# Kernel tuning notes

Hardware: AMD Instinct MI355X
Metric: run time of the kernel (lower is better)

Reference implementation:

```python
import jax, jax.numpy as jnp
import numpy as np

# dMoE config (matches init_kwargs): D=1024, GLU ffn F=2816 (int(2*4096/3) rounded up to 256),
# E=8 experts, top_k=2, erf-GELU activation, normalize_expert_weights=0 (skip), bias added to output.
D = 1024
F = 2816
E = 8
TOP_K = 2


def setup_inputs() -> dict:
    key = jax.random.key(0)
    ks = jax.random.split(key, 6)
    std = 0.02
    x = jax.random.normal(ks[0], (2, 2048, D), dtype=jnp.float32)
    router_w = jax.random.normal(ks[1], (D, E), dtype=jnp.float32) * std
    w1 = jax.random.normal(ks[2], (E, D, F), dtype=jnp.float32) * std
    v1 = jax.random.normal(ks[3], (E, D, F), dtype=jnp.float32) * std
    w2 = jax.random.normal(ks[4], (E, F, D), dtype=jnp.float32) * std
    bias = jnp.zeros((D,), dtype=jnp.float32)
    return {"x": x, "router_w": router_w, "w1": w1, "v1": v1, "w2": w2, "bias": bias}


def reference(x, router_w, w1, v1, w2, bias):
    B, S, d = x.shape
    xt = x.reshape(B * S, d)                       # [T, D] tokens
    # Router: linear -> softmax over experts -> top-k (no weight renormalization, p=0).
    scores = jax.nn.softmax(xt @ router_w, axis=-1)          # [T, E]
    expert_weights, expert_idx = jax.lax.top_k(scores, TOP_K)  # [T, k]
    # Dropless MoE == dense per-expert GLU MLP combined with top-k weights
    # (non-selected experts get weight 0, mathematically identical to dispatch/combine).
    h = jax.nn.gelu(jnp.einsum('td,edf->tef', xt, w1), approximate=False) \
        * jnp.einsum('td,edf->tef', xt, v1)                   # [T, E, F]
    y = jnp.einsum('tef,efd->ted', h, w2)                     # [T, E, D]
    yk = jnp.take_along_axis(y, expert_idx[:, :, None], axis=1)  # [T, k, D]
    out = jnp.sum(expert_weights[:, :, None] * yk, axis=1) + bias
    return out.reshape(B, S, d)
```

## Files before the change

kernel.cpp:

```cpp
#include <hip/hip_runtime.h>
#include <hip/hip_bf16.h>
#include <math.h>

#define D_DIM 1024
#define F_DIM 2816
#define E_NUM 8

#define BM 128
#define BK 64

typedef __attribute__((ext_vector_type(4))) float f32x4;
typedef __attribute__((ext_vector_type(8))) short short8;

__device__ __forceinline__ unsigned short f2bf(float f) {
    unsigned u = __float_as_uint(f);
    u = (u + 0x7FFFu + ((u >> 16) & 1u)) >> 16;
    return (unsigned short)u;
}

__device__ __forceinline__ float gelu_erf(float z) {
    return 0.5f * z * (1.0f + erff(z * 0.70710678118654752f));
}

__device__ __forceinline__ int swz(int row, int kb) {
    return row * 128 + (kb ^ ((row & 7) << 4));
}

__device__ __forceinline__ uint4 pack8(const unsigned short* h) {
    uint4 r;
    r.x = (unsigned)h[0] | ((unsigned)h[1] << 16);
    r.y = (unsigned)h[2] | ((unsigned)h[3] << 16);
    r.z = (unsigned)h[4] | ((unsigned)h[5] << 16);
    r.w = (unsigned)h[6] | ((unsigned)h[7] << 16);
    return r;
}

__device__ __forceinline__ void gload16(const void* g, void* l) {
    __builtin_amdgcn_global_load_lds(
        (const __attribute__((address_space(1))) unsigned int*)g,
        (__attribute__((address_space(3))) unsigned int*)l,
        16, 0, 0);
}

__global__ __launch_bounds__(256) void transpose_cvt_kernel(
    const float* __restrict__ src, unsigned short* __restrict__ dst, int R, int C)
{
    __shared__ float tile[64][65];
    int e = blockIdx.z;
    const float* s = src + (size_t)e * R * C;
    unsigned short* d = dst + (size_t)e * R * C;
    int c0 = blockIdx.x * 64;
    int r0 = blockIdx.y * 64;
    int tid = threadIdx.x;
#pragma unroll
    for (int i = 0; i < 4; ++i) {
        int idx = tid + 256 * i;
        int r = idx >> 4, cc = (idx & 15) * 4;
        float4 v = *(const float4*)(s + (size_t)(r0 + r) * C + c0 + cc);
        tile[r][cc] = v.x; tile[r][cc + 1] = v.y; tile[r][cc + 2] = v.z; tile[r][cc + 3] = v.w;
    }
    __syncthreads();
#pragma unroll
    for (int i = 0; i < 2; ++i) {
        int idx = tid + 256 * i;
        int c = idx >> 3, rr = (idx & 7) * 8;
        unsigned short h[8];
#pragma unroll
        for (int j = 0; j < 8; ++j) h[j] = f2bf(tile[rr + j][c]);
        *(uint4*)(d + (size_t)(c0 + c) * R + r0 + rr) = pack8(h);
    }
}

__global__ __launch_bounds__(64) void router_kernel(
    const float* __restrict__ x, const float* __restrict__ rw,
    unsigned short* __restrict__ xbf, int* __restrict__ tk_idx,
    float* __restrict__ tk_w, int* __restrict__ counts)
{
    int t = blockIdx.x;
    int lane = threadIdx.x;
    const float* xr = x + (size_t)t * D_DIM;
    float acc[E_NUM];
#pragma unroll
    for (int e = 0; e < E_NUM; ++e) acc[e] = 0.f;
#pragma unroll
    for (int i = 0; i < D_DIM / 64; ++i) {
        int d = lane + 64 * i;
        float xv = xr[d];
        xbf[(size_t)t * D_DIM + d] = f2bf(xv);
        const float* rp = rw + (size_t)d * E_NUM;
#pragma unroll
        for (int e = 0; e < E_NUM; ++e) acc[e] += xv * rp[e];
    }
#pragma unroll
    for (int e = 0; e < E_NUM; ++e) {
#pragma unroll
        for (int s = 32; s > 0; s >>= 1) acc[e] += __shfl_xor(acc[e], s, 64);
    }
    float mx = acc[0];
#pragma unroll
    for (int e = 1; e < E_NUM; ++e) mx = fmaxf(mx, acc[e]);
    float p[E_NUM], se = 0.f;
#pragma unroll
    for (int e = 0; e < E_NUM; ++e) { p[e] = expf(acc[e] - mx); se += p[e]; }
    float inv = 1.f / se;
    int e1 = 0;
#pragma unroll
    for (int e = 1; e < E_NUM; ++e) if (p[e] > p[e1]) e1 = e;
    int e2 = (e1 == 0) ? 1 : 0;
#pragma unroll
    for (int e = 0; e < E_NUM; ++e) if (e != e1 && p[e] > p[e2]) e2 = e;
    if (lane == 0) {
        tk_idx[2 * t] = e1; tk_idx[2 * t + 1] = e2;
        tk_w[2 * t] = p[e1] * inv; tk_w[2 * t + 1] = p[e2] * inv;
        atomicAdd(&counts[e1], 1);
        atomicAdd(&counts[e2], 1);
    }
}

__global__ void scan_kernel(const int* __restrict__ counts, int* __restrict__ offsets,
                            int* __restrict__ tile_e, int* __restrict__ tile_row,
                            int* __restrict__ n_mt)
{
    if (threadIdx.x != 0) return;
    int off = 0, nt = 0;
    for (int e = 0; e < E_NUM; ++e) {
        offsets[e] = off;
        int ne = counts[e];
        int nti = (ne + BM - 1) / BM;
        for (int i = 0; i < nti; ++i) { tile_e[nt] = e; tile_row[nt] = off + i * BM; ++nt; }
        off += ne;
    }
    offsets[E_NUM] = off;
    *n_mt = nt;
}

__global__ __launch_bounds__(256) void compact_kernel(
    const int* __restrict__ tk_idx, const int* __restrict__ offsets,
    int* __restrict__ pair_token, int* __restrict__ pair_pos, int T)
{
    int e = blockIdx.x;
    int tid = threadIdx.x;
    __shared__ int s[256];
    __shared__ int running;
    if (tid == 0) running = 0;
    __syncthreads();
    int base0 = offsets[e];
    for (int base = 0; base < T; base += 256) {
        int t = base + tid;
        int flag = 0, slot = -1;
        if (t < T) {
            int i0 = tk_idx[2 * t], i1 = tk_idx[2 * t + 1];
            slot = (i0 == e) ? 0 : ((i1 == e) ? 1 : -1);
            flag = (slot >= 0) ? 1 : 0;
        }
        s[tid] = flag;
        __syncthreads();
        for (int d = 1; d < 256; d <<= 1) {
            int v = (tid >= d) ? s[tid - d] : 0;
            __syncthreads();
            s[tid] += v;
            __syncthreads();
        }
        int total = s[255];
        int run = running;
        if (flag) {
            int pos = base0 + run + s[tid] - 1;
            pair_token[pos] = t;
            pair_pos[2 * t + slot] = pos;
        }
        __syncthreads();
        if (tid == 0) running += total;
        __syncthreads();
    }
}

__global__ __launch_bounds__(512) void gemm1_glu_kernel(
    const unsigned short* __restrict__ xbf,
    const unsigned short* __restrict__ w1t, const unsigned short* __restrict__ v1t,
    const int* __restrict__ pair_token, const int* __restrict__ offsets,
    const int* __restrict__ tile_e, const int* __restrict__ tile_row,
    const int* __restrict__ n_mt,
    unsigned short* __restrict__ hbf)
{
    int mt = blockIdx.x;
    if (mt >= *n_mt) return;
    int e = tile_e[mt];
    int row0 = tile_row[mt];
    int end = offsets[e + 1];
    int n0 = blockIdx.y * 64;

    __shared__ __align__(16) unsigned short As[BM * BK];
    __shared__ __align__(16) unsigned short B0s[64 * BK];
    __shared__ __align__(16) unsigned short B1s[64 * BK];

    int tid = threadIdx.x;
    int lane = tid & 63;
    int wid = tid >> 6;
    int wr = wid >> 1, wc = wid & 1;
    int sub = lane >> 3;
    int srcoff = (((lane & 7) ^ sub) << 4);

    const unsigned short* W0 = w1t + (size_t)e * D_DIM * F_DIM;
    const unsigned short* W1 = v1t + (size_t)e * D_DIM * F_DIM;

    const char* aptr[2];
#pragma unroll
    for (int i = 0; i < 2; ++i) {
        int row = (wid * 2 + i) * 8 + sub;
        int p = row0 + row;
        if (p >= end) p = end - 1;
        aptr[i] = (const char*)(xbf + (size_t)pair_token[p] * D_DIM) + srcoff;
    }
    int nb = wid * 8 + sub;
    const char* b0ptr = (const char*)(W0 + (size_t)(n0 + nb) * D_DIM) + srcoff;
    const char* b1ptr = (const char*)(W1 + (size_t)(n0 + nb) * D_DIM) + srcoff;

    f32x4 acc[2][2][2];
#pragma unroll
    for (int a = 0; a < 2; ++a)
#pragma unroll
        for (int m = 0; m < 2; ++m)
#pragma unroll
            for (int n = 0; n < 2; ++n) acc[a][m][n] = (f32x4){0.f, 0.f, 0.f, 0.f};

    auto STAGE = [&]() {
#pragma unroll
        for (int i = 0; i < 2; ++i) {
            gload16(aptr[i], (char*)As + (wid * 2 + i) * 1024);
            aptr[i] += 128;
        }
        gload16(b0ptr, (char*)B0s + wid * 1024);
        b0ptr += 128;
        gload16(b1ptr, (char*)B1s + wid * 1024);
        b1ptr += 128;
    };

    const int NT = D_DIM / BK;
    for (int kt = 0; kt < NT; ++kt) {
        STAGE();
        __syncthreads();
#pragma unroll
        for (int kk = 0; kk < 2; ++kk) {
            int kb = kk * 64 + (lane >> 4) * 16;
            short8 af[2];
#pragma unroll
            for (int m = 0; m < 2; ++m) {
                int row = wr * 32 + m * 16 + (lane & 15);
                af[m] = *(const short8*)((char*)As + swz(row, kb));
            }
            short8 bf0[2], bf1[2];
#pragma unroll
            for (int n = 0; n < 2; ++n) {
                int rn = wc * 32 + n * 16 + (lane & 15);
                bf0[n] = *(const short8*)((char*)B0s + swz(rn, kb));
                bf1[n] = *(const short8*)((char*)B1s + swz(rn, kb));
            }
#pragma unroll
            for (int m = 0; m < 2; ++m)
#pragma unroll
                for (int n = 0; n < 2; ++n) {
                    acc[0][m][n] = __builtin_amdgcn_mfma_f32_16x16x32_bf16(af[m], bf0[n], acc[0][m][n], 0, 0, 0);
                    acc[1][m][n] = __builtin_amdgcn_mfma_f32_16x16x32_bf16(af[m], bf1[n], acc[1][m][n], 0, 0, 0);
                }
        }
        __syncthreads();
    }
#pragma unroll
    for (int m = 0; m < 2; ++m) {
#pragma unroll
        for (int j = 0; j < 4; ++j) {
            int rl = wr * 32 + m * 16 + (lane >> 4) * 4 + j;
            int p = row0 + rl;
            if (p < end) {
#pragma unroll
                for (int n = 0; n < 2; ++n) {
                    float z1 = acc[0][m][n][j];
                    float z2 = acc[1][m][n][j];
                    float hv = gelu_erf(z1) * z2;
                    hbf[(size_t)p * F_DIM + n0 + wc * 32 + n * 16 + (lane & 15)] = f2bf(hv);
                }
            }
        }
    }
}

__global__ __launch_bounds__(512) void gemm2_kernel(
    const unsigned short* __restrict__ hbf,
    const unsigned short* __restrict__ w2t,
    const int* __restrict__ offsets,
    const int* __restrict__ tile_e, const int* __restrict__ tile_row,
    const int* __restrict__ n_mt,
    float* __restrict__ ypair)
{
    int mt = blockIdx.x;
    if (mt >= *n_mt) return;
    int e = tile_e[mt];
    int row0 = tile_row[mt];
    int end = offsets[e + 1];
    int n0 = blockIdx.y * 128;

    __shared__ __align__(16) unsigned short As[BM * BK];
    __shared__ __align__(16) unsigned short Bs[128 * BK];

    int tid = threadIdx.x;
    int lane = tid & 63;
    int wid = tid >> 6;
    int wr = wid >> 2, wc = wid & 3;
    int sub = lane >> 3;
    int srcoff = (((lane & 7) ^ sub) << 4);

    const unsigned short* W = w2t + (size_t)e * D_DIM * F_DIM;

    const char* aptr[2];
#pragma unroll
    for (int i = 0; i < 2; ++i) {
        int row = (wid * 2 + i) * 8 + sub;
        int p = row0 + row;
        if (p >= end) p = end - 1;
        aptr[i] = (const char*)(hbf + (size_t)p * F_DIM) + srcoff;
    }
    const char* bptr[2];
#pragma unroll
    for (int i = 0; i < 2; ++i) {
        int n = (wid * 2 + i) * 8 + sub;
        bptr[i] = (const char*)(W + (size_t)(n0 + n) * F_DIM) + srcoff;
    }

    f32x4 acc[4][2];
#pragma unroll
    for (int m = 0; m < 4; ++m)
#pragma unroll
        for (int n = 0; n < 2; ++n) acc[m][n] = (f32x4){0.f, 0.f, 0.f, 0.f};

    auto STAGE = [&]() {
#pragma unroll
        for (int i = 0; i < 2; ++i) {
            gload16(aptr[i], (char*)As + (wid * 2 + i) * 1024);
            aptr[i] += 128;
            gload16(bptr[i], (char*)Bs + (wid * 2 + i) * 1024);
            bptr[i] += 128;
        }
    };

    const int NT = F_DIM / BK;
    for (int kt = 0; kt < NT; ++kt) {
        STAGE();
        __syncthreads();
#pragma unroll
        for (int kk = 0; kk < 2; ++kk) {
            int kb = kk * 64 + (lane >> 4) * 16;
            short8 af[4];
#pragma unroll
            for (int m = 0; m < 4; ++m) {
                int row = wr * 64 + m * 16 + (lane & 15);
                af[m] = *(const short8*)((char*)As + swz(row, kb));
            }
            short8 bfr[2];
#pragma unroll
            for (int n = 0; n < 2; ++n) {
                int rn = wc * 32 + n * 16 + (lane & 15);
                bfr[n] = *(const short8*)((char*)Bs + swz(rn, kb));
            }
#pragma unroll
            for (int m = 0; m < 4; ++m)
#pragma unroll
                for (int n = 0; n < 2; ++n)
                    acc[m][n] = __builtin_amdgcn_mfma_f32_16x16x32_bf16(af[m], bfr[n], acc[m][n], 0, 0, 0);
        }
        __syncthreads();
    }
#pragma unroll
    for (int m = 0; m < 4; ++m) {
#pragma unroll
        for (int j = 0; j < 4; ++j) {
            int rl = wr * 64 + m * 16 + (lane >> 4) * 4 + j;
            int p = row0 + rl;
            if (p < end) {
#pragma unroll
                for (int n = 0; n < 2; ++n)
                    ypair[(size_t)p * D_DIM + n0 + wc * 32 + n * 16 + (lane & 15)] = acc[m][n][j];
            }
        }
    }
}

__global__ __launch_bounds__(256) void combine_kernel(
    const float* __restrict__ ypair, const int* __restrict__ pair_pos,
    const float* __restrict__ tk_w, const float* __restrict__ bias,
    float* __restrict__ out, int total)
{
    int idx = blockIdx.x * 256 + threadIdx.x;
    if (idx >= total) return;
    int t = idx >> 10;
    int d = idx & (D_DIM - 1);
    int p0 = pair_pos[2 * t], p1 = pair_pos[2 * t + 1];
    float r = bias[d] + tk_w[2 * t] * ypair[(size_t)p0 * D_DIM + d]
                      + tk_w[2 * t + 1] * ypair[(size_t)p1 * D_DIM + d];
    out[idx] = r;
}

__global__ void ws_too_small_kernel(float* out, int n) {
    int i = blockIdx.x * 256 + threadIdx.x;
    if (i < n) out[i] = 12345.0f;
}

extern "C" void kernel_launch(void* const* d_in, const int* in_sizes, int n_in,
                              void* d_out, int out_size, void* d_ws, size_t ws_size,
                              hipStream_t stream) {
    const float* x    = (const float*)d_in[0];
    const float* rw   = (const float*)d_in[1];
    const float* w1   = (const float*)d_in[2];
    const float* v1   = (const float*)d_in[3];
    const float* w2   = (const float*)d_in[4];
    const float* bias = (const float*)d_in[5];
    float* out = (float*)d_out;

    int T = in_sizes[0] / D_DIM;
    int P = 2 * T;
    int maxMT = P / BM + E_NUM;

    char* p = (char*)d_ws;
    char* ws_end = p + ws_size;
    auto alloc = [&](size_t bytes) {
        char* r = p;
        p += (bytes + 255) & ~(size_t)255;
        return r;
    };
    unsigned short* xbf   = (unsigned short*)alloc((size_t)T * D_DIM * 2);
    int*   tk_idx     = (int*)alloc((size_t)T * 2 * 4);
    float* tk_w       = (float*)alloc((size_t)T * 2 * 4);
    int*   counts     = (int*)alloc(E_NUM * 4);
    int*   offsets    = (int*)alloc((E_NUM + 1) * 4);
    int*   tile_e     = (int*)alloc(maxMT * 4);
    int*   tile_row   = (int*)alloc(maxMT * 4);
    int*   n_mt       = (int*)alloc(4);
    int*   pair_token = (int*)alloc((size_t)P * 4);
    int*   pair_pos   = (int*)alloc((size_t)P * 4);
    unsigned short* hbf = (unsigned short*)alloc((size_t)P * F_DIM * 2);
    float* ypair      = (float*)alloc((size_t)P * D_DIM * 4);
    unsigned short* w1t = (unsigned short*)alloc((size_t)E_NUM * D_DIM * F_DIM * 2);
    unsigned short* v1t = (unsigned short*)alloc((size_t)E_NUM * D_DIM * F_DIM * 2);
    unsigned short* w2t = (unsigned short*)alloc((size_t)E_NUM * D_DIM * F_DIM * 2);

    if (p > ws_end) {
        ws_too_small_kernel<<<(out_size + 255) / 256, 256, 0, stream>>>(out, out_size);
        return;
    }

    hipMemsetAsync(counts, 0, E_NUM * 4, stream);
    transpose_cvt_kernel<<<dim3(F_DIM / 64, D_DIM / 64, E_NUM), 256, 0, stream>>>(w1, w1t, D_DIM, F_DIM);
    transpose_cvt_kernel<<<dim3(F_DIM / 64, D_DIM / 64, E_NUM), 256, 0, stream>>>(v1, v1t, D_DIM, F_DIM);
    transpose_cvt_kernel<<<dim3(D_DIM / 64, F_DIM / 64, E_NUM), 256, 0, stream>>>(w2, w2t, F_DIM, D_DIM);
    router_kernel<<<T, 64, 0, stream>>>(x, rw, xbf, tk_idx, tk_w, counts);
    scan_kernel<<<1, 64, 0, stream>>>(counts, offsets, tile_e, tile_row, n_mt);
    compact_kernel<<<E_NUM, 256, 0, stream>>>(tk_idx, offsets, pair_token, pair_pos, T);
    gemm1_glu_kernel<<<dim3(maxMT, F_DIM / 64), 512, 0, stream>>>(
        xbf, w1t, v1t, pair_token, offsets, tile_e, tile_row, n_mt, hbf);
    gemm2_kernel<<<dim3(maxMT, D_DIM / 128), 512, 0, stream>>>(
        hbf, w2t, offsets, tile_e, tile_row, n_mt, ypair);
    combine_kernel<<<(T * D_DIM + 255) / 256, 256, 0, stream>>>(
        ypair, pair_pos, tk_w, bias, out, T * D_DIM);
}
```

Before: 456.2 us.

## Double-buffer GEMM LDS tiles and fuse top-k combine into GEMM2 via atomics

Both expert GEMM kernels now double-buffer their shared-memory tiles. The next K-slice load is issued before computing on the current one, which removes one barrier per iteration and overlaps global loads with MFMA work. The separate combine kernel and the ypair buffer are replaced: a bias-init kernel writes the bias into the output, and GEMM2 scales each result by its routing weight and atomically adds it into the token's output row. This removes the fp32 ypair write and read-back, at the cost of doubled LDS use (possibly lower occupancy) and global float atomics with a nondeterministic summation order.

```diff
diff --git a/kernel.cpp b/kernel.cpp
--- a/kernel.cpp
+++ b/kernel.cpp
@@ -136,7 +136,8 @@
 
 __global__ __launch_bounds__(256) void compact_kernel(
     const int* __restrict__ tk_idx, const int* __restrict__ offsets,
-    int* __restrict__ pair_token, int* __restrict__ pair_pos, int T)
+    const float* __restrict__ tk_w,
+    int* __restrict__ pair_token, float* __restrict__ pair_w, int T)
 {
     int e = blockIdx.x;
     int tid = threadIdx.x;
@@ -166,12 +167,21 @@
         if (flag) {
             int pos = base0 + run + s[tid] - 1;
             pair_token[pos] = t;
-            pair_pos[2 * t + slot] = pos;
+            pair_w[pos] = tk_w[2 * t + slot];
         }
         __syncthreads();
         if (tid == 0) running += total;
         __syncthreads();
     }
+}
+
+__global__ __launch_bounds__(256) void bias_init_kernel(
+    const float* __restrict__ bias, float* __restrict__ out, int total4)
+{
+    int idx = blockIdx.x * 256 + threadIdx.x;
+    if (idx >= total4) return;
+    int d4 = idx & (D_DIM / 4 - 1);
+    ((float4*)out)[idx] = ((const float4*)bias)[d4];
 }
 
 __global__ __launch_bounds__(512) void gemm1_glu_kernel(
@@ -189,9 +199,9 @@
     int end = offsets[e + 1];
     int n0 = blockIdx.y * 64;
 
-    __shared__ __align__(16) unsigned short As[BM * BK];
-    __shared__ __align__(16) unsigned short B0s[64 * BK];
-    __shared__ __align__(16) unsigned short B1s[64 * BK];
+    __shared__ __align__(16) unsigned short As[2][BM * BK];
+    __shared__ __align__(16) unsigned short B0s[2][64 * BK];
+    __shared__ __align__(16) unsigned short B1s[2][64 * BK];
 
     int tid = threadIdx.x;
     int lane = tid & 63;
@@ -223,22 +233,27 @@
 #pragma unroll
             for (int n = 0; n < 2; ++n) acc[a][m][n] = (f32x4){0.f, 0.f, 0.f, 0.f};
 
-    auto STAGE = [&]() {
+    auto STAGE = [&](int buf) {
 #pragma unroll
         for (int i = 0; i < 2; ++i) {
-            gload16(aptr[i], (char*)As + (wid * 2 + i) * 1024);
+            gload16(aptr[i], (char*)As[buf] + (wid * 2 + i) * 1024);
             aptr[i] += 128;
         }
-        gload16(b0ptr, (char*)B0s + wid * 1024);
+        gload16(b0ptr, (char*)B0s[buf] + wid * 1024);
         b0ptr += 128;
-        gload16(b1ptr, (char*)B1s + wid * 1024);
+        gload16(b1ptr, (char*)B1s[buf] + wid * 1024);
         b1ptr += 128;
     };
 
+    STAGE(0);
     const int NT = D_DIM / BK;
+    int cur = 0;
     for (int kt = 0; kt < NT; ++kt) {
-        STAGE();
         __syncthreads();
+        if (kt + 1 < NT) STAGE(cur ^ 1);
+        const char* Ab = (const char*)As[cur];
+        const char* B0b = (const char*)B0s[cur];
+        const char* B1b = (const char*)B1s[cur];
 #pragma unroll
         for (int kk = 0; kk < 2; ++kk) {
             int kb = kk * 64 + (lane >> 4) * 16;
@@ -246,14 +261,14 @@
 #pragma unroll
             for (int m = 0; m < 2; ++m) {
                 int row = wr * 32 + m * 16 + (lane & 15);
-                af[m] = *(const short8*)((char*)As + swz(row, kb));
+                af[m] = *(const short8*)(Ab + swz(row, kb));
             }
             short8 bf0[2], bf1[2];
 #pragma unroll
             for (int n = 0; n < 2; ++n) {
                 int rn = wc * 32 + n * 16 + (lane & 15);
-                bf0[n] = *(const short8*)((char*)B0s + swz(rn, kb));
-                bf1[n] = *(const short8*)((char*)B1s + swz(rn, kb));
+                bf0[n] = *(const short8*)(B0b + swz(rn, kb));
+                bf1[n] = *(const short8*)(B1b + swz(rn, kb));
             }
 #pragma unroll
             for (int m = 0; m < 2; ++m)
@@ -263,7 +278,7 @@
                     acc[1][m][n] = __builtin_amdgcn_mfma_f32_16x16x32_bf16(af[m], bf1[n], acc[1][m][n], 0, 0, 0);
                 }
         }
-        __syncthreads();
+        cur ^= 1;
     }
 #pragma unroll
     for (int m = 0; m < 2; ++m) {
@@ -290,7 +305,8 @@
     const int* __restrict__ offsets,
     const int* __restrict__ tile_e, const int* __restrict__ tile_row,
     const int* __restrict__ n_mt,
-    float* __restrict__ ypair)
+    const int* __restrict__ pair_token, const float* __restrict__ pair_w,
+    float* __restrict__ out)
 {
     int mt = blockIdx.x;
     if (mt >= *n_mt) return;
@@ -299,8 +315,8 @@
     int end = offsets[e + 1];
     int n0 = blockIdx.y * 128;
 
-    __shared__ __align__(16) unsigned short As[BM * BK];
-    __shared__ __align__(16) unsigned short Bs[128 * BK];
+    __shared__ __align__(16) unsigned short As[2][BM * BK];
+    __shared__ __align__(16) unsigned short Bs[2][128 * BK];
 
     int tid = threadIdx.x;
     int lane = tid & 63;
@@ -332,20 +348,24 @@
 #pragma unroll
         for (int n = 0; n < 2; ++n) acc[m][n] = (f32x4){0.f, 0.f, 0.f, 0.f};
 
-    auto STAGE = [&]() {
+    auto STAGE = [&](int buf) {
 #pragma unroll
         for (int i = 0; i < 2; ++i) {
-            gload16(aptr[i], (char*)As + (wid * 2 + i) * 1024);
+            gload16(aptr[i], (char*)As[buf] + (wid * 2 + i) * 1024);
             aptr[i] += 128;
-            gload16(bptr[i], (char*)Bs + (wid * 2 + i) * 1024);
+            gload16(bptr[i], (char*)Bs[buf] + (wid * 2 + i) * 1024);
             bptr[i] += 128;
         }
     };
 
+    STAGE(0);
     const int NT = F_DIM / BK;
+    int cur = 0;
     for (int kt = 0; kt < NT; ++kt) {
-        STAGE();
         __syncthreads();
+        if (kt + 1 < NT) STAGE(cur ^ 1);
+        const char* Ab = (const char*)As[cur];
+        const char* Bb = (const char*)Bs[cur];
 #pragma unroll
         for (int kk = 0; kk < 2; ++kk) {
             int kb = kk * 64 + (lane >> 4) * 16;
@@ -353,13 +373,13 @@
 #pragma unroll
             for (int m = 0; m < 4; ++m) {
                 int row = wr * 64 + m * 16 + (lane & 15);
-                af[m] = *(const short8*)((char*)As + swz(row, kb));
+                af[m] = *(const short8*)(Ab + swz(row, kb));
             }
             short8 bfr[2];
 #pragma unroll
             for (int n = 0; n < 2; ++n) {
                 int rn = wc * 32 + n * 16 + (lane & 15);
-                bfr[n] = *(const short8*)((char*)Bs + swz(rn, kb));
+                bfr[n] = *(const short8*)(Bb + swz(rn, kb));
             }
 #pragma unroll
             for (int m = 0; m < 4; ++m)
@@ -367,7 +387,7 @@
                 for (int n = 0; n < 2; ++n)
                     acc[m][n] = __builtin_amdgcn_mfma_f32_16x16x32_bf16(af[m], bfr[n], acc[m][n], 0, 0, 0);
         }
-        __syncthreads();
+        cur ^= 1;
     }
 #pragma unroll
     for (int m = 0; m < 4; ++m) {
@@ -376,27 +396,15 @@
             int rl = wr * 64 + m * 16 + (lane >> 4) * 4 + j;
             int p = row0 + rl;
             if (p < end) {
+                int t = pair_token[p];
+                float w = pair_w[p];
+                float* orow = out + (size_t)t * D_DIM + n0 + wc * 32 + (lane & 15);
 #pragma unroll
                 for (int n = 0; n < 2; ++n)
-                    ypair[(size_t)p * D_DIM + n0 + wc * 32 + n * 16 + (lane & 15)] = acc[m][n][j];
-            }
-        }
-    }
-}
-
-__global__ __launch_bounds__(256) void combine_kernel(
-    const float* __restrict__ ypair, const int* __restrict__ pair_pos,
-    const float* __restrict__ tk_w, const float* __restrict__ bias,
-    float* __restrict__ out, int total)
-{
-    int idx = blockIdx.x * 256 + threadIdx.x;
-    if (idx >= total) return;
-    int t = idx >> 10;
-    int d = idx & (D_DIM - 1);
-    int p0 = pair_pos[2 * t], p1 = pair_pos[2 * t + 1];
-    float r = bias[d] + tk_w[2 * t] * ypair[(size_t)p0 * D_DIM + d]
-                      + tk_w[2 * t + 1] * ypair[(size_t)p1 * D_DIM + d];
-    out[idx] = r;
+                    atomicAdd(orow + n * 16, w * acc[m][n][j]);
+            }
+        }
+    }
 }
 
 __global__ void ws_too_small_kernel(float* out, int n) {
@@ -435,9 +443,8 @@
     int*   tile_row   = (int*)alloc(maxMT * 4);
     int*   n_mt       = (int*)alloc(4);
     int*   pair_token = (int*)alloc((size_t)P * 4);
-    int*   pair_pos   = (int*)alloc((size_t)P * 4);
+    float* pair_w     = (float*)alloc((size_t)P * 4);
     unsigned short* hbf = (unsigned short*)alloc((size_t)P * F_DIM * 2);
-    float* ypair      = (float*)alloc((size_t)P * D_DIM * 4);
     unsigned short* w1t = (unsigned short*)alloc((size_t)E_NUM * D_DIM * F_DIM * 2);
     unsigned short* v1t = (unsigned short*)alloc((size_t)E_NUM * D_DIM * F_DIM * 2);
     unsigned short* w2t = (unsigned short*)alloc((size_t)E_NUM * D_DIM * F_DIM * 2);
@@ -453,11 +460,10 @@
     transpose_cvt_kernel<<<dim3(D_DIM / 64, F_DIM / 64, E_NUM), 256, 0, stream>>>(w2, w2t, F_DIM, D_DIM);
     router_kernel<<<T, 64, 0, stream>>>(x, rw, xbf, tk_idx, tk_w, counts);
     scan_kernel<<<1, 64, 0, stream>>>(counts, offsets, tile_e, tile_row, n_mt);
-    compact_kernel<<<E_NUM, 256, 0, stream>>>(tk_idx, offsets, pair_token, pair_pos, T);
+    compact_kernel<<<E_NUM, 256, 0, stream>>>(tk_idx, offsets, tk_w, pair_token, pair_w, T);
     gemm1_glu_kernel<<<dim3(maxMT, F_DIM / 64), 512, 0, stream>>>(
         xbf, w1t, v1t, pair_token, offsets, tile_e, tile_row, n_mt, hbf);
+    bias_init_kernel<<<(T * D_DIM / 4 + 255) / 256, 256, 0, stream>>>(bias, out, T * D_DIM / 4);
     gemm2_kernel<<<dim3(maxMT, D_DIM / 128), 512, 0, stream>>>(
-        hbf, w2t, offsets, tile_e, tile_row, n_mt, ypair);
-    combine_kernel<<<(T * D_DIM + 255) / 256, 256, 0, stream>>>(
-        ypair, pair_pos, tk_w, bias, out, T * D_DIM);
-}
+        hbf, w2t, offsets, tile_e, tile_row, n_mt, pair_token, pair_w, out);
+}
```

Measured after the change: 493.2 us. +8.1%, slower.

## Enlarge MoE GEMM tiles to 256 rows with double-buffered LDS and XCD-aware block remap

Applied to the files above, without the earlier changes.

Both grouped GEMMs move to 256-row M tiles. The GLU GEMM now computes a 128-wide combined w1/v1 N strip per block, and each wave holds a larger accumulator set. LDS is double-buffered, with loads issued two stages ahead and explicit vmcnt waits and barriers replacing the single-buffer syncthreads loop. Block indices are remapped so consecutive logical tiles go to the same XCD to improve L2 reuse. The aim is more reuse per load and latency hiding, at the cost of higher register and LDS pressure (lower occupancy) and more wasted work on partially filled expert tiles.

```diff
diff --git a/kernel.cpp b/kernel.cpp
--- a/kernel.cpp
+++ b/kernel.cpp
@@ -6,7 +6,7 @@
 #define F_DIM 2816
 #define E_NUM 8
 
-#define BM 128
+#define BM 256
 #define BK 64
 
 typedef __attribute__((ext_vector_type(4))) float f32x4;
@@ -182,102 +182,125 @@
     const int* __restrict__ n_mt,
     unsigned short* __restrict__ hbf)
 {
-    int mt = blockIdx.x;
+    __shared__ __align__(16) unsigned short As[2][256 * BK];
+    __shared__ __align__(16) unsigned short Bs[2][256 * BK];
+
+    int flat = blockIdx.x + gridDim.x * blockIdx.y;
+    int nwg = gridDim.x * gridDim.y;
+    int L = (flat & 7) * (nwg >> 3) + (flat >> 3);
+    int mt = L % gridDim.x;
+    int strip = L / gridDim.x;
     if (mt >= *n_mt) return;
     int e = tile_e[mt];
     int row0 = tile_row[mt];
     int end = offsets[e + 1];
-    int n0 = blockIdx.y * 64;
-
-    __shared__ __align__(16) unsigned short As[BM * BK];
-    __shared__ __align__(16) unsigned short B0s[64 * BK];
-    __shared__ __align__(16) unsigned short B1s[64 * BK];
+    int n0 = strip * 128;
 
     int tid = threadIdx.x;
     int lane = tid & 63;
     int wid = tid >> 6;
-    int wr = wid >> 1, wc = wid & 1;
+    int wr = wid >> 2, wc = wid & 3;
     int sub = lane >> 3;
     int srcoff = (((lane & 7) ^ sub) << 4);
 
     const unsigned short* W0 = w1t + (size_t)e * D_DIM * F_DIM;
     const unsigned short* W1 = v1t + (size_t)e * D_DIM * F_DIM;
 
-    const char* aptr[2];
-#pragma unroll
-    for (int i = 0; i < 2; ++i) {
-        int row = (wid * 2 + i) * 8 + sub;
-        int p = row0 + row;
+    const char* aptr[4];
+#pragma unroll
+    for (int i = 0; i < 4; ++i) {
+        int r = (wid * 4 + i) * 8 + sub;
+        int p = row0 + r;
         if (p >= end) p = end - 1;
         aptr[i] = (const char*)(xbf + (size_t)pair_token[p] * D_DIM) + srcoff;
     }
-    int nb = wid * 8 + sub;
-    const char* b0ptr = (const char*)(W0 + (size_t)(n0 + nb) * D_DIM) + srcoff;
-    const char* b1ptr = (const char*)(W1 + (size_t)(n0 + nb) * D_DIM) + srcoff;
-
-    f32x4 acc[2][2][2];
-#pragma unroll
-    for (int a = 0; a < 2; ++a)
-#pragma unroll
-        for (int m = 0; m < 2; ++m)
-#pragma unroll
-            for (int n = 0; n < 2; ++n) acc[a][m][n] = (f32x4){0.f, 0.f, 0.f, 0.f};
-
-    auto STAGE = [&]() {
-#pragma unroll
-        for (int i = 0; i < 2; ++i) {
-            gload16(aptr[i], (char*)As + (wid * 2 + i) * 1024);
+    const char* bptr[4];
+#pragma unroll
+    for (int i = 0; i < 4; ++i) {
+        int gb = wid * 4 + i;
+        int g = gb >> 3;
+        int s = (gb >> 2) & 1;
+        int u = (gb & 3) * 8 + sub;
+        int col = n0 + g * 32 + u;
+        const unsigned short* base = s ? W1 : W0;
+        bptr[i] = (const char*)(base + (size_t)col * D_DIM) + srcoff;
+    }
+
+    f32x4 acc[8][4];
+#pragma unroll
+    for (int m = 0; m < 8; ++m)
+#pragma unroll
+        for (int n = 0; n < 4; ++n) acc[m][n] = (f32x4){0.f, 0.f, 0.f, 0.f};
+
+    auto STAGE = [&](int buf) {
+#pragma unroll
+        for (int i = 0; i < 4; ++i) {
+            gload16(aptr[i], (char*)As[buf] + (wid * 4 + i) * 1024);
             aptr[i] += 128;
         }
-        gload16(b0ptr, (char*)B0s + wid * 1024);
-        b0ptr += 128;
-        gload16(b1ptr, (char*)B1s + wid * 1024);
-        b1ptr += 128;
+#pragma unroll
+        for (int i = 0; i < 4; ++i) {
+            gload16(bptr[i], (char*)Bs[buf] + (wid * 4 + i) * 1024);
+            bptr[i] += 128;
+        }
     };
 
+    STAGE(0);
+    STAGE(1);
     const int NT = D_DIM / BK;
+#pragma unroll 1
     for (int kt = 0; kt < NT; ++kt) {
-        STAGE();
-        __syncthreads();
-#pragma unroll
-        for (int kk = 0; kk < 2; ++kk) {
-            int kb = kk * 64 + (lane >> 4) * 16;
-            short8 af[2];
-#pragma unroll
-            for (int m = 0; m < 2; ++m) {
-                int row = wr * 32 + m * 16 + (lane & 15);
-                af[m] = *(const short8*)((char*)As + swz(row, kb));
+        int cur = kt & 1;
+        if (kt + 1 < NT) asm volatile("s_waitcnt vmcnt(8)" ::: "memory");
+        else             asm volatile("s_waitcnt vmcnt(0)" ::: "memory");
+        __builtin_amdgcn_s_barrier();
+        __builtin_amdgcn_sched_barrier(0);
+        const char* Ab = (const char*)As[cur];
+        const char* Bb = (const char*)Bs[cur];
+        short8 bf[4][2];
+#pragma unroll
+        for (int nf = 0; nf < 4; ++nf)
+#pragma unroll
+            for (int kk = 0; kk < 2; ++kk) {
+                int rn = wc * 64 + nf * 16 + (lane & 15);
+                bf[nf][kk] = *(const short8*)(Bb + swz(rn, kk * 64 + (lane >> 4) * 16));
             }
-            short8 bf0[2], bf1[2];
-#pragma unroll
-            for (int n = 0; n < 2; ++n) {
-                int rn = wc * 32 + n * 16 + (lane & 15);
-                bf0[n] = *(const short8*)((char*)B0s + swz(rn, kb));
-                bf1[n] = *(const short8*)((char*)B1s + swz(rn, kb));
-            }
-#pragma unroll
-            for (int m = 0; m < 2; ++m)
-#pragma unroll
-                for (int n = 0; n < 2; ++n) {
-                    acc[0][m][n] = __builtin_amdgcn_mfma_f32_16x16x32_bf16(af[m], bf0[n], acc[0][m][n], 0, 0, 0);
-                    acc[1][m][n] = __builtin_amdgcn_mfma_f32_16x16x32_bf16(af[m], bf1[n], acc[1][m][n], 0, 0, 0);
+#pragma unroll
+        for (int q = 0; q < 4; ++q) {
+            short8 af[2][2];
+#pragma unroll
+            for (int i = 0; i < 2; ++i)
+#pragma unroll
+                for (int kk = 0; kk < 2; ++kk) {
+                    int row = wr * 128 + (q * 2 + i) * 16 + (lane & 15);
+                    af[i][kk] = *(const short8*)(Ab + swz(row, kk * 64 + (lane >> 4) * 16));
                 }
-        }
-        __syncthreads();
-    }
-#pragma unroll
-    for (int m = 0; m < 2; ++m) {
+#pragma unroll
+            for (int i = 0; i < 2; ++i)
+#pragma unroll
+                for (int nf = 0; nf < 4; ++nf)
+#pragma unroll
+                    for (int kk = 0; kk < 2; ++kk)
+                        acc[q * 2 + i][nf] = __builtin_amdgcn_mfma_f32_16x16x32_bf16(
+                            af[i][kk], bf[nf][kk], acc[q * 2 + i][nf], 0, 0, 0);
+        }
+        __builtin_amdgcn_sched_barrier(0);
+        __builtin_amdgcn_s_barrier();
+        if (kt + 2 < NT) STAGE(cur);
+    }
+#pragma unroll
+    for (int m = 0; m < 8; ++m) {
 #pragma unroll
         for (int j = 0; j < 4; ++j) {
-            int rl = wr * 32 + m * 16 + (lane >> 4) * 4 + j;
+            int rl = wr * 128 + m * 16 + (lane >> 4) * 4 + j;
             int p = row0 + rl;
             if (p < end) {
 #pragma unroll
-                for (int n = 0; n < 2; ++n) {
-                    float z1 = acc[0][m][n][j];
-                    float z2 = acc[1][m][n][j];
-                    float hv = gelu_erf(z1) * z2;
-                    hbf[(size_t)p * F_DIM + n0 + wc * 32 + n * 16 + (lane & 15)] = f2bf(hv);
+                for (int nf = 0; nf < 2; ++nf) {
+                    float z1 = acc[m][nf][j];
+                    float z2 = acc[m][nf + 2][j];
+                    int col = n0 + wc * 32 + nf * 16 + (lane & 15);
+                    hbf[(size_t)p * F_DIM + col] = f2bf(gelu_erf(z1) * z2);
                 }
             }
         }
@@ -292,30 +315,34 @@
     const int* __restrict__ n_mt,
     float* __restrict__ ypair)
 {
-    int mt = blockIdx.x;
+    __shared__ __align__(16) unsigned short As[2][256 * BK];
+    __shared__ __align__(16) unsigned short Bs[2][128 * BK];
+
+    int flat = blockIdx.x + gridDim.x * blockIdx.y;
+    int nwg = gridDim.x * gridDim.y;
+    int L = (flat & 7) * (nwg >> 3) + (flat >> 3);
+    int mt = L % gridDim.x;
+    int strip = L / gridDim.x;
     if (mt >= *n_mt) return;
     int e = tile_e[mt];
     int row0 = tile_row[mt];
     int end = offsets[e + 1];
-    int n0 = blockIdx.y * 128;
-
-    __shared__ __align__(16) unsigned short As[BM * BK];
-    __shared__ __align__(16) unsigned short Bs[128 * BK];
+    int n0 = strip * 128;
 
     int tid = threadIdx.x;
     int lane = tid & 63;
     int wid = tid >> 6;
-    int wr = wid >> 2, wc = wid & 3;
+    int wr = wid >> 1, wc = wid & 1;
     int sub = lane >> 3;
     int srcoff = (((lane & 7) ^ sub) << 4);
 
     const unsigned short* W = w2t + (size_t)e * D_DIM * F_DIM;
 
-    const char* aptr[2];
-#pragma unroll
-    for (int i = 0; i < 2; ++i) {
-        int row = (wid * 2 + i) * 8 + sub;
-        int p = row0 + row;
+    const char* aptr[4];
+#pragma unroll
+    for (int i = 0; i < 4; ++i) {
+        int r = (wid * 4 + i) * 8 + sub;
+        int p = row0 + r;
         if (p >= end) p = end - 1;
         aptr[i] = (const char*)(hbf + (size_t)p * F_DIM) + srcoff;
     }
@@ -326,48 +353,67 @@
         bptr[i] = (const char*)(W + (size_t)(n0 + n) * F_DIM) + srcoff;
     }
 
-    f32x4 acc[4][2];
+    f32x4 acc[4][4];
 #pragma unroll
     for (int m = 0; m < 4; ++m)
 #pragma unroll
-        for (int n = 0; n < 2; ++n) acc[m][n] = (f32x4){0.f, 0.f, 0.f, 0.f};
-
-    auto STAGE = [&]() {
+        for (int n = 0; n < 4; ++n) acc[m][n] = (f32x4){0.f, 0.f, 0.f, 0.f};
+
+    auto STAGE = [&](int buf) {
+#pragma unroll
+        for (int i = 0; i < 4; ++i) {
+            gload16(aptr[i], (char*)As[buf] + (wid * 4 + i) * 1024);
+            aptr[i] += 128;
+        }
 #pragma unroll
         for (int i = 0; i < 2; ++i) {
-            gload16(aptr[i], (char*)As + (wid * 2 + i) * 1024);
-            aptr[i] += 128;
-            gload16(bptr[i], (char*)Bs + (wid * 2 + i) * 1024);
+            gload16(bptr[i], (char*)Bs[buf] + (wid * 2 + i) * 1024);
             bptr[i] += 128;
         }
     };
 
+    STAGE(0);
+    STAGE(1);
     const int NT = F_DIM / BK;
+#pragma unroll 1
     for (int kt = 0; kt < NT; ++kt) {
-        STAGE();
-        __syncthreads();
-#pragma unroll
-        for (int kk = 0; kk < 2; ++kk) {
-            int kb = kk * 64 + (lane >> 4) * 16;
-            short8 af[4];
-#pragma unroll
-            for (int m = 0; m < 4; ++m) {
-                int row = wr * 64 + m * 16 + (lane & 15);
-                af[m] = *(const short8*)((char*)As + swz(row, kb));
+        int cur = kt & 1;
+        if (kt + 1 < NT) asm volatile("s_waitcnt vmcnt(6)" ::: "memory");
+        else             asm volatile("s_waitcnt vmcnt(0)" ::: "memory");
+        __builtin_amdgcn_s_barrier();
+        __builtin_amdgcn_sched_barrier(0);
+        const char* Ab = (const char*)As[cur];
+        const char* Bb = (const char*)Bs[cur];
+        short8 bf[4][2];
+#pragma unroll
+        for (int nf = 0; nf < 4; ++nf)
+#pragma unroll
+            for (int kk = 0; kk < 2; ++kk) {
+                int rn = wc * 64 + nf * 16 + (lane & 15);
+                bf[nf][kk] = *(const short8*)(Bb + swz(rn, kk * 64 + (lane >> 4) * 16));
             }
-            short8 bfr[2];
-#pragma unroll
-            for (int n = 0; n < 2; ++n) {
-                int rn = wc * 32 + n * 16 + (lane & 15);
-                bfr[n] = *(const short8*)((char*)Bs + swz(rn, kb));
-            }
-#pragma unroll
-            for (int m = 0; m < 4; ++m)
-#pragma unroll
-                for (int n = 0; n < 2; ++n)
-                    acc[m][n] = __builtin_amdgcn_mfma_f32_16x16x32_bf16(af[m], bfr[n], acc[m][n], 0, 0, 0);
-        }
-        __syncthreads();
+#pragma unroll
+        for (int q = 0; q < 2; ++q) {
+            short8 af[2][2];
+#pragma unroll
+            for (int i = 0; i < 2; ++i)
+#pragma unroll
+                for (int kk = 0; kk < 2; ++kk) {
+                    int row = wr * 64 + (q * 2 + i) * 16 + (lane & 15);
+                    af[i][kk] = *(const short8*)(Ab + swz(row, kk * 64 + (lane >> 4) * 16));
+                }
+#pragma unroll
+            for (int i = 0; i < 2; ++i)
+#pragma unroll
+                for (int nf = 0; nf < 4; ++nf)
+#pragma unroll
+                    for (int kk = 0; kk < 2; ++kk)
+                        acc[q * 2 + i][nf] = __builtin_amdgcn_mfma_f32_16x16x32_bf16(
+                            af[i][kk], bf[nf][kk], acc[q * 2 + i][nf], 0, 0, 0);
+        }
+        __builtin_amdgcn_sched_barrier(0);
+        __builtin_amdgcn_s_barrier();
+        if (kt + 2 < NT) STAGE(cur);
     }
 #pragma unroll
     for (int m = 0; m < 4; ++m) {
@@ -377,8 +423,8 @@
             int p = row0 + rl;
             if (p < end) {
 #pragma unroll
-                for (int n = 0; n < 2; ++n)
-                    ypair[(size_t)p * D_DIM + n0 + wc * 32 + n * 16 + (lane & 15)] = acc[m][n][j];
+                for (int nf = 0; nf < 4; ++nf)
+                    ypair[(size_t)p * D_DIM + n0 + wc * 64 + nf * 16 + (lane & 15)] = acc[m][nf][j];
             }
         }
     }
@@ -454,7 +500,7 @@
     router_kernel<<<T, 64, 0, stream>>>(x, rw, xbf, tk_idx, tk_w, counts);
     scan_kernel<<<1, 64, 0, stream>>>(counts, offsets, tile_e, tile_row, n_mt);
     compact_kernel<<<E_NUM, 256, 0, stream>>>(tk_idx, offsets, pair_token, pair_pos, T);
-    gemm1_glu_kernel<<<dim3(maxMT, F_DIM / 64), 512, 0, stream>>>(
+    gemm1_glu_kernel<<<dim3(maxMT, (2 * F_DIM) / 256), 512, 0, stream>>>(
         xbf, w1t, v1t, pair_token, offsets, tile_e, tile_row, n_mt, hbf);
     gemm2_kernel<<<dim3(maxMT, D_DIM / 128), 512, 0, stream>>>(
         hbf, w2t, offsets, tile_e, tile_row, n_mt, ypair);
```

Result: slower. 490.0 us (+7.4%).
